# Kernel optimization log

Hardware: AMD Instinct MI355X
Metric: run time of the kernel (lower is better)

The kernel has to match this reference:

```python
import jax, jax.numpy as jnp
import numpy as np

N_HIDDEN = 2048
D_IN = 64
T_STEPS = 4096
WASHOUT = 200
SPECTRAL_RADIUS = 0.9
RIDGE_LAMBDA = 1e-6


def _scale_to_spectral_radius(W, rho, iters=100):
    # power iteration to estimate the dominant eigenvalue magnitude (spectral radius)
    rng = np.random.default_rng(0)
    v = rng.normal(size=W.shape[0]).astype(np.float64)
    v /= np.linalg.norm(v)
    for _ in range(iters):
        w = W @ v
        nrm = np.linalg.norm(w)
        v = w / nrm
    rad = np.linalg.norm(W @ v)
    return W * (rho / rad)


def setup_inputs() -> dict:
    key = jax.random.key(0)
    k1, k2, k3, k4 = jax.random.split(key, 4)
    u = jax.random.normal(k1, (T_STEPS, D_IN), dtype=jnp.float32)
    y = jax.random.normal(k2, (T_STEPS, 1), dtype=jnp.float32)
    W_in = jax.random.normal(k3, (N_HIDDEN, D_IN), dtype=jnp.float32) * 0.1
    W = np.asarray(jax.random.normal(k4, (N_HIDDEN, N_HIDDEN), dtype=jnp.float32), dtype=np.float64)
    W /= np.sqrt(N_HIDDEN)
    W = _scale_to_spectral_radius(W, SPECTRAL_RADIUS)
    W_res = jnp.asarray(W, dtype=jnp.float32)
    return {"u": u, "y": y, "W_in": W_in, "W_res": W_res, "washout": WASHOUT}


def reference(u, y, W_in, W_res, washout):
    # precompute input drive W_in @ u[t] for all t: [T, N]
    drive = u @ W_in.T
    x0 = jnp.zeros((W_res.shape[0],), dtype=u.dtype)

    def step(x, d):
        x = jnp.tanh(W_res @ x + d)
        return x, x

    _, X = jax.lax.scan(step, x0, drive)  # X: [T, N]
    Xw = X[washout:]                      # [T - washout, N]
    yw = y[washout:]                      # [T - washout, 1]
    A = Xw.T @ Xw + RIDGE_LAMBDA * jnp.eye(Xw.shape[1], dtype=Xw.dtype)
    Wout = jnp.linalg.solve(A, Xw.T @ yw)  # [N, 1]
    return Xw @ Wout                       # [T - washout, 1]
```

## Files before the change

### kernel.cpp

```cpp
#include <hip/hip_runtime.h>
#include <math.h>

#define NH      2048
#define TT      4096
#define DIN     64
#define WASH    200
#define TW      (TT - WASH)
#define LAMBDA  1e-6f

#define CG_BLOCKS    64
#define CG_ITERS     256
#define NTILE        528
#define NWORK        192

typedef unsigned long long u64;

#define X_OFF      ((size_t)0)
#define DRIVE_OFF  ((size_t)TT * NH)
#define A_OFF      DRIVE_OFF
#define B_OFF      ((size_t)2 * TT * NH)
#define WS_FLOATS  (B_OFF + NH)
#define XPACK_OFF  ((size_t)0)
#define ZPACK_OFF  ((size_t)2 * NH)
#define PQSLOT_OFF ((size_t)3 * NH)
#define RZSLOT_OFF ((size_t)3 * NH + 64)
#define U64_TOTAL  ((size_t)3 * NH + 128)

__device__ __forceinline__ u64 pack_ev(int epoch, float v) {
    return ((u64)(unsigned)epoch << 32) | (u64)__float_as_uint(v);
}
__device__ __forceinline__ int   ep_of(u64 p)  { return (int)(p >> 32); }
__device__ __forceinline__ float val_of(u64 p) { return __uint_as_float((unsigned)p); }
__device__ __forceinline__ u64 pack2f(float lo, float hi) {
    return ((u64)__float_as_uint(hi) << 32) | (u64)__float_as_uint(lo);
}
__device__ __forceinline__ float lo_of(u64 p) { return __uint_as_float((unsigned)p); }
__device__ __forceinline__ float hi_of(u64 p) { return __uint_as_float((unsigned)(p >> 32)); }

__device__ __forceinline__ u64 aload(const u64* p) {
    return __hip_atomic_load(p, __ATOMIC_RELAXED, __HIP_MEMORY_SCOPE_AGENT);
}
__device__ __forceinline__ void astore(u64* p, u64 v) {
    __hip_atomic_store(p, v, __ATOMIC_RELAXED, __HIP_MEMORY_SCOPE_AGENT);
}

__global__ void init_kernel(float* ws) {
    int tid = threadIdx.x;
    u64* ub = (u64*)(ws + WS_FLOATS);
    for (size_t i = tid; i < U64_TOTAL; i += 256) ub[i] = 0ull;
    for (int i = tid; i < NH; i += 256) ws[B_OFF + i] = 0.f;
}

__global__ __launch_bounds__(256) void drive_kernel(
    const float* __restrict__ u, const float* __restrict__ Win,
    float* __restrict__ drive)
{
    __shared__ float Wt[256 * 64];
    const int tid = threadIdx.x;
    const int ic = blockIdx.x & 7;
    const int tc = blockIdx.x >> 3;
    const int i0 = ic * 256;
    for (int idx = tid; idx < 256 * 64; idx += 256) {
        int il = idx >> 6, k = idx & 63;
        Wt[k * 256 + il] = Win[(size_t)i0 * 64 + idx];
    }
    __syncthreads();
    for (int tt_ = 0; tt_ < 128; ++tt_) {
        int t = tc * 128 + tt_;
        const float* ur = u + (size_t)t * DIN;
        float acc = 0.f;
        #pragma unroll
        for (int k = 0; k < 64; ++k)
            acc = fmaf(Wt[k * 256 + tid], ur[k], acc);
        drive[(size_t)t * NH + i0 + tid] = acc;
    }
}

__global__ __launch_bounds__(1024, 1) void scan_gram_kernel(
    const float* __restrict__ W, const float* __restrict__ drive,
    float* __restrict__ X, u64* xpack, float* __restrict__ A)
{
    __shared__ float xls[NH];
    __shared__ float As[16][64];
    __shared__ float Bs[16][64];
    const int tid = threadIdx.x;

    if (blockIdx.x < 64) {
        const int wave = tid >> 6;
        const int lane = tid & 63;
        const int rowA = blockIdx.x * 32 + wave * 2;

        float4 wA[8], wB[8];
        {
            const float* wpA = W + (size_t)rowA * NH + lane * 4;
            const float* wpB = wpA + NH;
            #pragma unroll
            for (int j = 0; j < 8; ++j) {
                wA[j] = *(const float4*)(wpA + 256 * j);
                wB[j] = *(const float4*)(wpB + 256 * j);
            }
        }

        for (int t = 0; t < TT; ++t) {
            float2 dv = {0.f, 0.f};
            if (lane == 0) dv = *(const float2*)&drive[(size_t)t * NH + rowA];

            if (t == 0) {
                xls[tid] = 0.f; xls[tid + 1024] = 0.f;
            } else {
                const u64* src = xpack + (size_t)((t - 1) & 1) * NH;
                const int want = t;
                u64 a = aload(&src[tid]);
                u64 b = aload(&src[tid + 1024]);
                bool pa = true, pb = true;
                if (ep_of(a) >= want) { xls[tid] = val_of(a); pa = false; }
                if (ep_of(b) >= want) { xls[tid + 1024] = val_of(b); pb = false; }
                while (pa || pb) {
                    __builtin_amdgcn_s_sleep(1);
                    if (pa) { u64 v = aload(&src[tid]);
                              if (ep_of(v) >= want) { xls[tid] = val_of(v); pa = false; } }
                    if (pb) { u64 v = aload(&src[tid + 1024]);
                              if (ep_of(v) >= want) { xls[tid + 1024] = val_of(v); pb = false; } }
                }
            }
            __syncthreads();

            float a0 = 0.f, a1 = 0.f;
            #pragma unroll
            for (int j = 0; j < 8; ++j) {
                float4 xv = *(const float4*)&xls[lane * 4 + 256 * j];
                float4 va = wA[j], vb = wB[j];
                a0 = fmaf(va.x, xv.x, fmaf(va.y, xv.y, fmaf(va.z, xv.z, fmaf(va.w, xv.w, a0))));
                a1 = fmaf(vb.x, xv.x, fmaf(vb.y, xv.y, fmaf(vb.z, xv.z, fmaf(vb.w, xv.w, a1))));
            }
            #pragma unroll
            for (int m = 32; m; m >>= 1) { a0 += __shfl_xor(a0, m); a1 += __shfl_xor(a1, m); }

            if (lane == 0) {
                float v0 = tanhf(a0 + dv.x);
                float v1 = tanhf(a1 + dv.y);
                astore((u64*)&X[(size_t)t * NH + rowA], pack2f(v0, v1));
                u64* dst = xpack + (size_t)(t & 1) * NH;
                astore(&dst[rowA],     pack_ev(t + 1, v0));
                astore(&dst[rowA + 1], pack_ev(t + 1, v1));
            }
            __syncthreads();
        }
        __threadfence();
        if (lane == 0) {
            u64* dst = xpack + (size_t)(TT & 1) * NH;
            astore(&dst[rowA],     pack_ev(TT + 1, 0.f));
            astore(&dst[rowA + 1], pack_ev(TT + 1, 0.f));
        }
    } else {
        const int wid = blockIdx.x - 64;
        int ti0[3], tj0[3]; int nt = 0;
        for (int L = wid; L < NTILE; L += NWORK) {
            int rem = L, a = 0;
            while (rem >= 32 - a) { rem -= 32 - a; ++a; }
            ti0[nt] = a * 64; tj0[nt] = (a + rem) * 64; ++nt;
        }
        float4 acc4[3] = {};
        const int ty = tid >> 5, tx = tid & 31;
        const u64* Xp = (const u64*)X;

        const int nch = (TW + 15) / 16;
        for (int ch = 0; ch < nch; ++ch) {
            const int tb = WASH + ch * 16;
            const int te = (tb + 15 < TT) ? tb + 15 : TT - 1;
            const int want = te + 2;
            const u64* buf = xpack + (size_t)((te + 1) & 1) * NH;
            if (tid < nt * 128) {
                int tt_ = tid >> 7, local = tid & 127;
                int base = (local & 64) ? tj0[tt_] : ti0[tt_];
                int r = base + (local & 63);
                u64 v = aload(&buf[r]);
                while (ep_of(v) < want) { __builtin_amdgcn_s_sleep(64); v = aload(&buf[r]); }
            }
            __syncthreads();

            for (int tt_ = 0; tt_ < nt; ++tt_) {
                const int i0 = ti0[tt_], j0 = tj0[tt_];
                {
                    int v = tid & 511;
                    int kk = v >> 5, c2 = v & 31;
                    int t = tb + kk;
                    int base = (tid < 512) ? i0 : j0;
                    float lo = 0.f, hi = 0.f;
                    if (t < TT) {
                        u64 w_ = aload(&Xp[((size_t)t * NH + base) / 2 + c2]);
                        lo = lo_of(w_); hi = hi_of(w_);
                    }
                    float* Sh = (tid < 512) ? &As[kk][c2 * 2] : &Bs[kk][c2 * 2];
                    Sh[0] = lo; Sh[1] = hi;
                }
                __syncthreads();
                float4 a = acc4[tt_];
                #pragma unroll
                for (int k = 0; k < 16; ++k) {
                    float2 av = *(const float2*)&As[k][ty * 2];
                    float2 bv2 = *(const float2*)&Bs[k][tx * 2];
                    a.x = fmaf(av.x, bv2.x, a.x); a.y = fmaf(av.x, bv2.y, a.y);
                    a.z = fmaf(av.y, bv2.x, a.z); a.w = fmaf(av.y, bv2.y, a.w);
                }
                acc4[tt_] = a;
                __syncthreads();
            }
        }
        for (int tt_ = 0; tt_ < nt; ++tt_) {
            const int i0 = ti0[tt_], j0 = tj0[tt_];
            const bool diag = (i0 == j0);
            float4 a = acc4[tt_];
            float vals[2][2] = {{a.x, a.y}, {a.z, a.w}};
            #pragma unroll
            for (int aa = 0; aa < 2; ++aa) {
                int gi = i0 + ty * 2 + aa;
                #pragma unroll
                for (int bb = 0; bb < 2; ++bb) {
                    int gj = j0 + tx * 2 + bb;
                    float v = vals[aa][bb];
                    if (gi == gj) v += LAMBDA;
                    A[(size_t)gi * NH + gj] = v;
                    if (!diag) A[(size_t)gj * NH + gi] = v;
                }
            }
        }
    }
}

__global__ void bvec_kernel(const float* __restrict__ X, const float* __restrict__ y,
                            float* __restrict__ bv)
{
    const int ic = blockIdx.x & 7, tc = blockIdx.x >> 3;
    const int i = ic * 256 + threadIdx.x;
    const int t0 = WASH + tc * (TW / 8), t1 = t0 + (TW / 8);
    float acc = 0.f;
    for (int t = t0; t < t1; ++t)
        acc = fmaf(X[(size_t)t * NH + i], y[t], acc);
    atomicAdd(&bv[i], acc);
}

__global__ __launch_bounds__(1024, 1) void cg_kernel(
    const float* __restrict__ A, const float* __restrict__ bvec,
    const float* __restrict__ X, float* __restrict__ out,
    u64* zpack, u64* pqslot, u64* rzslot)
{
    __shared__ float pls[NH];
    __shared__ float zls[NH];
    __shared__ float r32[32], x32[32], q32[32], inv32[32];
    __shared__ float csh[2];
    const int tid     = threadIdx.x;
    const int r_local = tid >> 5;
    const int lane32  = tid & 31;
    const int row0 = blockIdx.x * 32;
    const int row  = row0 + r_local;

    float4 areg[16];
    {
        const float* ap = A + (size_t)row * NH + lane32 * 4;
        #pragma unroll
        for (int j = 0; j < 16; ++j) areg[j] = *(const float4*)(ap + 128 * j);
    }

    pls[tid] = 0.f; pls[tid + 1024] = 0.f;

    if (tid < 32) {
        int i = row0 + tid;
        float bi = bvec[i];
        float iv = 1.0f / A[(size_t)i * NH + i];
        inv32[tid] = iv;
        x32[tid] = 0.f; r32[tid] = bi;
        float zi = iv * bi;
        astore(&zpack[i], pack_ev(1, zi));
        float part = bi * zi;
        #pragma unroll
        for (int m = 16; m; m >>= 1) part += __shfl_xor(part, m, 32);
        if (tid == 0) astore(&rzslot[blockIdx.x], pack_ev(1, part));
    }
    __syncthreads();

    float rho_prev = 1.f;

    for (int it = 0; it < CG_ITERS; ++it) {
        {
            const int want = it + 1;
            u64 a = aload(&zpack[tid]);
            u64 b = aload(&zpack[tid + 1024]);
            bool pa = true, pb = true;
            if (ep_of(a) >= want) { zls[tid] = val_of(a); pa = false; }
            if (ep_of(b) >= want) { zls[tid + 1024] = val_of(b); pb = false; }
            while (pa || pb) {
                __builtin_amdgcn_s_sleep(1);
                if (pa) { u64 v = aload(&zpack[tid]);
                          if (ep_of(v) >= want) { zls[tid] = val_of(v); pa = false; } }
                if (pb) { u64 v = aload(&zpack[tid + 1024]);
                          if (ep_of(v) >= want) { zls[tid + 1024] = val_of(v); pb = false; } }
            }
        }
        if (tid < 64) {
            u64 v = aload(&rzslot[tid]);
            while (ep_of(v) < it + 1) { __builtin_amdgcn_s_sleep(1); v = aload(&rzslot[tid]); }
            float s = val_of(v);
            #pragma unroll
            for (int m = 32; m; m >>= 1) s += __shfl_xor(s, m);
            if (tid == 0) csh[1] = s;
        }
        __syncthreads();
        float rho = csh[1];
        float beta = (it == 0) ? 0.f : ((rho_prev != 0.f) ? rho / rho_prev : 0.f);

        pls[tid]        = fmaf(beta, pls[tid],        zls[tid]);
        pls[tid + 1024] = fmaf(beta, pls[tid + 1024], zls[tid + 1024]);
        __syncthreads();

        float acc = 0.f;
        #pragma unroll
        for (int j = 0; j < 16; ++j) {
            float4 pv = *(const float4*)&pls[lane32 * 4 + 128 * j];
            float4 av = areg[j];
            acc = fmaf(av.x, pv.x, fmaf(av.y, pv.y,
                  fmaf(av.z, pv.z, fmaf(av.w, pv.w, acc))));
        }
        #pragma unroll
        for (int m = 16; m; m >>= 1) acc += __shfl_xor(acc, m, 32);
        if (lane32 == 0) q32[r_local] = acc;
        __syncthreads();

        if (tid < 32) {
            float t1 = q32[tid] * pls[row0 + tid];
            #pragma unroll
            for (int m = 16; m; m >>= 1) t1 += __shfl_xor(t1, m, 32);
            if (tid == 0) astore(&pqslot[blockIdx.x], pack_ev(it + 1, t1));
        }
        if (tid < 64) {
            u64 v = aload(&pqslot[tid]);
            while (ep_of(v) < it + 1) { __builtin_amdgcn_s_sleep(1); v = aload(&pqslot[tid]); }
            float s = val_of(v);
            #pragma unroll
            for (int m = 32; m; m >>= 1) s += __shfl_xor(s, m);
            if (tid == 0) csh[0] = s;
        }
        __syncthreads();
        float pq = csh[0];
        float alpha = (pq != 0.f) ? rho / pq : 0.f;

        if (tid < 32) {
            int i = row0 + tid;
            float pi = pls[i], qi = q32[tid];
            x32[tid] = fmaf(alpha, pi, x32[tid]);
            float ri = r32[tid] - alpha * qi;
            r32[tid] = ri;
            float zi = inv32[tid] * ri;
            astore(&zpack[i], pack_ev(it + 2, zi));
            float t2 = ri * zi;
            #pragma unroll
            for (int m = 16; m; m >>= 1) t2 += __shfl_xor(t2, m, 32);
            if (tid == 0) astore(&rzslot[blockIdx.x], pack_ev(it + 2, t2));
        }
        rho_prev = rho;
        __syncthreads();
    }

    if (tid < 32) {
        int i = row0 + tid;
        astore(&zpack[i], pack_ev(CG_ITERS + 2, x32[tid]));
    }
    {
        const int want = CG_ITERS + 2;
        u64 a = aload(&zpack[tid]);
        u64 b = aload(&zpack[tid + 1024]);
        bool pa = true, pb = true;
        if (ep_of(a) >= want) { zls[tid] = val_of(a); pa = false; }
        if (ep_of(b) >= want) { zls[tid + 1024] = val_of(b); pb = false; }
        while (pa || pb) {
            __builtin_amdgcn_s_sleep(1);
            if (pa) { u64 v = aload(&zpack[tid]);
                      if (ep_of(v) >= want) { zls[tid] = val_of(v); pa = false; } }
            if (pb) { u64 v = aload(&zpack[tid + 1024]);
                      if (ep_of(v) >= want) { zls[tid + 1024] = val_of(v); pb = false; } }
        }
    }
    __syncthreads();
    {
        const int i0r = (TW * (int)blockIdx.x) >> 6;
        const int i1r = (TW * ((int)blockIdx.x + 1)) >> 6;
        const int wave = tid >> 6, lane = tid & 63;
        for (int i = i0r + wave; i < i1r; i += 16) {
            const float* xr = X + (size_t)(WASH + i) * NH;
            float acc = 0.f;
            #pragma unroll
            for (int j = 0; j < 32; ++j)
                acc = fmaf(xr[j * 64 + lane], zls[j * 64 + lane], acc);
            #pragma unroll
            for (int m = 32; m; m >>= 1) acc += __shfl_xor(acc, m);
            if (lane == 0) out[i] = acc;
        }
    }
}

extern "C" void kernel_launch(void* const* d_in, const int* in_sizes, int n_in,
                              void* d_out, int out_size, void* d_ws, size_t ws_size,
                              hipStream_t stream)
{
    const float* u    = (const float*)d_in[0];
    const float* y    = (const float*)d_in[1];
    const float* Win  = (const float*)d_in[2];
    const float* Wres = (const float*)d_in[3];

    float* ws = (float*)d_ws;
    float* X     = ws + X_OFF;
    float* drive = ws + DRIVE_OFF;
    float* A     = ws + A_OFF;
    u64*   ub    = (u64*)(ws + WS_FLOATS);
    u64*   xpack  = ub + XPACK_OFF;
    u64*   zpack  = ub + ZPACK_OFF;
    u64*   pqslot = ub + PQSLOT_OFF;
    u64*   rzslot = ub + RZSLOT_OFF;

    init_kernel<<<1, 256, 0, stream>>>(ws);
    drive_kernel<<<256, 256, 0, stream>>>(u, Win, drive);
    scan_gram_kernel<<<256, 1024, 0, stream>>>(Wres, drive, X, xpack, A);
    bvec_kernel<<<64, 256, 0, stream>>>(X, y, ws + B_OFF);
    cg_kernel<<<CG_BLOCKS, 1024, 0, stream>>>(A, ws + B_OFF, X, (float*)d_out,
                                              zpack, pqslot, rzslot);
}
```

Baseline: 13.14 ms.

## Double-buffer scan shared state and fuse readout rhs into scan kernel

The scan loop now double-buffers the shared hidden-state vector, which lets it drop the trailing per-step block barrier, halving barriers on the serial recurrence critical path. The X^T y right-hand side is accumulated in registers by the scan lanes as each state is produced, replacing the separate bvec kernel, its re-read of X, and the atomic zeroing. Dropping the barrier relies on the two-buffer alternation being sufficient to avoid a fast wave overwriting a buffer still being read.

```diff
diff --git a/kernel.cpp b/kernel.cpp
--- a/kernel.cpp
+++ b/kernel.cpp
@@ -48,7 +48,6 @@
     int tid = threadIdx.x;
     u64* ub = (u64*)(ws + WS_FLOATS);
     for (size_t i = tid; i < U64_TOTAL; i += 256) ub[i] = 0ull;
-    for (int i = tid; i < NH; i += 256) ws[B_OFF + i] = 0.f;
 }
 
 __global__ __launch_bounds__(256) void drive_kernel(
@@ -78,9 +77,11 @@
 
 __global__ __launch_bounds__(1024, 1) void scan_gram_kernel(
     const float* __restrict__ W, const float* __restrict__ drive,
-    float* __restrict__ X, u64* xpack, float* __restrict__ A)
+    const float* __restrict__ y,
+    float* __restrict__ X, u64* xpack, float* __restrict__ A,
+    float* __restrict__ bv)
 {
-    __shared__ float xls[NH];
+    __shared__ float xls[2][NH];
     __shared__ float As[16][64];
     __shared__ float Bs[16][64];
     const int tid = threadIdx.x;
@@ -101,26 +102,29 @@
             }
         }
 
+        float b0 = 0.f, b1 = 0.f;
+
         for (int t = 0; t < TT; ++t) {
+            float* xb = xls[t & 1];
             float2 dv = {0.f, 0.f};
             if (lane == 0) dv = *(const float2*)&drive[(size_t)t * NH + rowA];
 
             if (t == 0) {
-                xls[tid] = 0.f; xls[tid + 1024] = 0.f;
+                xb[tid] = 0.f; xb[tid + 1024] = 0.f;
             } else {
                 const u64* src = xpack + (size_t)((t - 1) & 1) * NH;
                 const int want = t;
                 u64 a = aload(&src[tid]);
                 u64 b = aload(&src[tid + 1024]);
                 bool pa = true, pb = true;
-                if (ep_of(a) >= want) { xls[tid] = val_of(a); pa = false; }
-                if (ep_of(b) >= want) { xls[tid + 1024] = val_of(b); pb = false; }
+                if (ep_of(a) >= want) { xb[tid] = val_of(a); pa = false; }
+                if (ep_of(b) >= want) { xb[tid + 1024] = val_of(b); pb = false; }
                 while (pa || pb) {
                     __builtin_amdgcn_s_sleep(1);
                     if (pa) { u64 v = aload(&src[tid]);
-                              if (ep_of(v) >= want) { xls[tid] = val_of(v); pa = false; } }
+                              if (ep_of(v) >= want) { xb[tid] = val_of(v); pa = false; } }
                     if (pb) { u64 v = aload(&src[tid + 1024]);
-                              if (ep_of(v) >= want) { xls[tid + 1024] = val_of(v); pb = false; } }
+                              if (ep_of(v) >= want) { xb[tid + 1024] = val_of(v); pb = false; } }
                 }
             }
             __syncthreads();
@@ -128,7 +132,7 @@
             float a0 = 0.f, a1 = 0.f;
             #pragma unroll
             for (int j = 0; j < 8; ++j) {
-                float4 xv = *(const float4*)&xls[lane * 4 + 256 * j];
+                float4 xv = *(const float4*)&xb[lane * 4 + 256 * j];
                 float4 va = wA[j], vb = wB[j];
                 a0 = fmaf(va.x, xv.x, fmaf(va.y, xv.y, fmaf(va.z, xv.z, fmaf(va.w, xv.w, a0))));
                 a1 = fmaf(vb.x, xv.x, fmaf(vb.y, xv.y, fmaf(vb.z, xv.z, fmaf(vb.w, xv.w, a1))));
@@ -143,14 +147,20 @@
                 u64* dst = xpack + (size_t)(t & 1) * NH;
                 astore(&dst[rowA],     pack_ev(t + 1, v0));
                 astore(&dst[rowA + 1], pack_ev(t + 1, v1));
-            }
-            __syncthreads();
+                if (t >= WASH) {
+                    float yv = y[t];
+                    b0 = fmaf(v0, yv, b0);
+                    b1 = fmaf(v1, yv, b1);
+                }
+            }
         }
         __threadfence();
         if (lane == 0) {
             u64* dst = xpack + (size_t)(TT & 1) * NH;
             astore(&dst[rowA],     pack_ev(TT + 1, 0.f));
             astore(&dst[rowA + 1], pack_ev(TT + 1, 0.f));
+            bv[rowA]     = b0;
+            bv[rowA + 1] = b1;
         }
     } else {
         const int wid = blockIdx.x - 64;
@@ -228,18 +238,6 @@
     }
 }
 
-__global__ void bvec_kernel(const float* __restrict__ X, const float* __restrict__ y,
-                            float* __restrict__ bv)
-{
-    const int ic = blockIdx.x & 7, tc = blockIdx.x >> 3;
-    const int i = ic * 256 + threadIdx.x;
-    const int t0 = WASH + tc * (TW / 8), t1 = t0 + (TW / 8);
-    float acc = 0.f;
-    for (int t = t0; t < t1; ++t)
-        acc = fmaf(X[(size_t)t * NH + i], y[t], acc);
-    atomicAdd(&bv[i], acc);
-}
-
 __global__ __launch_bounds__(1024, 1) void cg_kernel(
     const float* __restrict__ A, const float* __restrict__ bvec,
     const float* __restrict__ X, float* __restrict__ out,
@@ -419,8 +417,8 @@
 
     init_kernel<<<1, 256, 0, stream>>>(ws);
     drive_kernel<<<256, 256, 0, stream>>>(u, Win, drive);
-    scan_gram_kernel<<<256, 1024, 0, stream>>>(Wres, drive, X, xpack, A);
-    bvec_kernel<<<64, 256, 0, stream>>>(X, y, ws + B_OFF);
+    scan_gram_kernel<<<256, 1024, 0, stream>>>(Wres, drive, y, X, xpack, A,
+                                               ws + B_OFF);
     cg_kernel<<<CG_BLOCKS, 1024, 0, stream>>>(A, ws + B_OFF, X, (float*)d_out,
                                               zpack, pqslot, rzslot);
 }
```

Measured after the change: 14.63 ms. +11.3%, slower.
